# Performance work log

Hardware: AMD Instinct MI355X
Metric: run time of the kernel (lower is better)

The kernel has to match this reference:

```python
import jax, jax.numpy as jnp
import numpy as np

B, S, D = 32, 1024, 512
LN_EPS = 1e-5


def setup_inputs() -> dict:
    key = jax.random.key(0)
    ks = jax.random.split(key, 12)
    scale = 1.0 / np.sqrt(D)
    return {
        "seq1": jax.random.normal(ks[0], (B, S, D), jnp.float32),
        "seq2": jax.random.normal(ks[1], (B, S, D), jnp.float32),
        "mask1": jax.random.randint(ks[2], (B, S), 0, 2) == 1,
        "mask2": jax.random.randint(ks[3], (B, S), 0, 2) == 1,
        "Wq": jax.random.uniform(ks[4], (D, D), jnp.float32, -scale, scale),
        "bq": jax.random.uniform(ks[5], (D,), jnp.float32, -scale, scale),
        "Wk": jax.random.uniform(ks[6], (D, D), jnp.float32, -scale, scale),
        "bk": jax.random.uniform(ks[7], (D,), jnp.float32, -scale, scale),
        "Wv": jax.random.uniform(ks[8], (D, D), jnp.float32, -scale, scale),
        "bv": jax.random.uniform(ks[9], (D,), jnp.float32, -scale, scale),
        "gamma": jnp.ones((D,), jnp.float32),
        "beta": jnp.zeros((D,), jnp.float32),
    }


def _layernorm(x, gamma, beta):
    mu = jnp.mean(x, axis=-1, keepdims=True)
    var = jnp.mean(jnp.square(x - mu), axis=-1, keepdims=True)
    return (x - mu) * jax.lax.rsqrt(var + LN_EPS) * gamma + beta


def reference(seq1, seq2, mask1, mask2, Wq, bq, Wk, bk, Wv, bv, gamma, beta):
    # relu-projected Q/K/V (shared weights across both sequences)
    q1 = jax.nn.relu(seq1 @ Wq + bq)
    k1 = jax.nn.relu(seq1 @ Wk + bk)
    v1 = jax.nn.relu(seq1 @ Wv + bv)
    q2 = jax.nn.relu(seq2 @ Wq + bq)
    k2 = jax.nn.relu(seq2 @ Wk + bk)
    v2 = jax.nn.relu(seq2 @ Wv + bv)

    # bilinear cross scores: tanh(k1 q2^T) summed over seq2 -> [B,S1]
    a1 = jnp.sum(jnp.tanh(jnp.einsum('bsd,btd->bst', k1, q2)), axis=2)
    a2 = jnp.sum(jnp.tanh(jnp.einsum('btd,bsd->bts', k2, q1)), axis=2)

    a1 = jnp.where(mask1, -jnp.inf, a1)
    a2 = jnp.where(mask2, -jnp.inf, a2)
    a1 = jax.nn.softmax(a1, axis=-1)  # [B,S1]
    a2 = jax.nn.softmax(a2, axis=-1)  # [B,S2]
    # dropout p=0.2 is identity at inference

    vector1 = jnp.einsum('bs,bsd->bd', a1, v1)
    vector2 = jnp.einsum('bs,bsd->bd', a2, v2)

    out1 = _layernorm(jnp.mean(seq1, axis=1) + vector1, gamma, beta)
    out2 = _layernorm(jnp.mean(seq2, axis=1) + vector2, gamma, beta)
    return (out1, out2)
```

## Files before the change

kernel.cpp:

```cpp
#include <hip/hip_runtime.h>


typedef __bf16 bf16x8_t __attribute__((ext_vector_type(8)));
typedef float f32x4_t __attribute__((ext_vector_type(4)));

__device__ __forceinline__ unsigned short f2bf(float f) {
    union { float f; unsigned int u; } c; c.f = f;
    unsigned int u = c.u;
    unsigned int r = (u + 0x7FFFu + ((u >> 16) & 1u)) >> 16;
    return (unsigned short)r;
}
__device__ __forceinline__ float bf2f(unsigned short h) {
    union { unsigned int u; float f; } c; c.u = ((unsigned int)h) << 16;
    return c.f;
}
__device__ __forceinline__ void gl2lds16(const void* g, void* l) {
    __builtin_amdgcn_global_load_lds(
        (const __attribute__((address_space(1))) void*)g,
        (__attribute__((address_space(3))) void*)l, 16, 0, 0);
}
__device__ __forceinline__ float fast_tanh(float x) {
    float e = __expf(2.f * x);
    return 1.f - 2.f * __builtin_amdgcn_rcpf(e + 1.f);
}

__global__ __launch_bounds__(256) void x2bf_kernel(
    const float* __restrict__ src, unsigned short* __restrict__ dst,
    float* __restrict__ accv)
{
    int chunk = blockIdx.x;
    int b = blockIdx.y;
    int tid = threadIdx.x, lane = tid & 63, wv = tid >> 6;
    __shared__ float red[4][512];
    float sum[8] = {};
    size_t base = ((size_t)b * 1024 + (size_t)chunk * 128) * 512;
    #pragma unroll 4
    for (int i = 0; i < 32; ++i) {
        int r = i * 4 + wv;
        size_t ro = base + (size_t)r * 512;
        float4 a = *reinterpret_cast<const float4*>(&src[ro + lane * 4]);
        float4 c = *reinterpret_cast<const float4*>(&src[ro + 256 + lane * 4]);
        ushort4 ha; ha.x = f2bf(a.x); ha.y = f2bf(a.y); ha.z = f2bf(a.z); ha.w = f2bf(a.w);
        ushort4 hc; hc.x = f2bf(c.x); hc.y = f2bf(c.y); hc.z = f2bf(c.z); hc.w = f2bf(c.w);
        *reinterpret_cast<ushort4*>(&dst[ro + lane * 4]) = ha;
        *reinterpret_cast<ushort4*>(&dst[ro + 256 + lane * 4]) = hc;
        sum[0] += a.x; sum[1] += a.y; sum[2] += a.z; sum[3] += a.w;
        sum[4] += c.x; sum[5] += c.y; sum[6] += c.z; sum[7] += c.w;
    }
    #pragma unroll
    for (int t = 0; t < 4; ++t) {
        red[wv][lane * 4 + t] = sum[t];
        red[wv][256 + lane * 4 + t] = sum[4 + t];
    }
    __syncthreads();
    #pragma unroll
    for (int j = 0; j < 2; ++j) {
        int col = tid + j * 256;
        float s = red[0][col] + red[1][col] + red[2][col] + red[3][col];
        atomicAdd(&accv[(size_t)b * 512 + col], s * (1.f / 1024.f));
    }
}

__global__ __launch_bounds__(256) void wconv_kernel(
    const float* __restrict__ Wq, const float* __restrict__ Wk,
    const float* __restrict__ Wv, unsigned short* __restrict__ Wt)
{
    const float* W = (blockIdx.z == 0) ? Wq : (blockIdx.z == 1) ? Wk : Wv;
    unsigned short* o = Wt + (size_t)blockIdx.z * 512 * 512;
    __shared__ unsigned short t[64][65];
    int k0 = blockIdx.x * 64, n0 = blockIdx.y * 64;
    #pragma unroll
    for (int i = 0; i < 16; ++i) {
        int idx = i * 256 + threadIdx.x;
        int r = idx >> 6, c = idx & 63;
        t[r][c] = f2bf(W[(size_t)(k0 + r) * 512 + n0 + c]);
    }
    __syncthreads();
    #pragma unroll
    for (int i = 0; i < 16; ++i) {
        int idx = i * 256 + threadIdx.x;
        int r = idx >> 6, c = idx & 63;
        o[(size_t)(n0 + r) * 512 + k0 + c] = t[c][r];
    }
}

__global__ __launch_bounds__(512) void biascat_kernel(
    const float* __restrict__ bq, const float* __restrict__ bk,
    const float* __restrict__ bv, float* __restrict__ bc)
{
    int n = threadIdx.x;
    bc[n] = bq[n]; bc[512 + n] = bk[n]; bc[1024 + n] = bv[n];
}

__global__ __launch_bounds__(256) void qkv_gemm(
    const unsigned short* __restrict__ Xb1, const unsigned short* __restrict__ Xb2,
    const unsigned short* __restrict__ Wt, const float* __restrict__ bias_cat,
    unsigned short* __restrict__ qkv)
{
    int nt = blockIdx.x;
    int mg = blockIdx.y;
    int z = mg >> 8;
    int m0 = (mg & 255) * 128;
    int n0 = nt * 128;

    const unsigned short* X = z ? Xb2 : Xb1;

    __shared__ alignas(16) unsigned char smem[128 * 136 * 2];
    unsigned short* As = (unsigned short*)smem;
    unsigned short* Bs = (unsigned short*)(smem + 8192);
    unsigned short* Ct = (unsigned short*)smem;

    int tid = threadIdx.x;
    int lane = tid & 63, wv = tid >> 6;
    int wm = wv >> 1, wn = wv & 1;
    int q = lane >> 4, ln = lane & 15;

    f32x4_t acc[4][4] = {};

    for (int k0 = 0; k0 < 512; k0 += 32) {
        #pragma unroll
        for (int j = 0; j < 2; ++j) {
            int cbase = j * 256 + wv * 64;
            int c = cbase + lane;
            int row = c >> 2, k8 = (c & 3) * 8;
            gl2lds16(&X[(size_t)(m0 + row) * 512 + k0 + k8], &As[cbase * 8]);
            gl2lds16(&Wt[(size_t)(n0 + row) * 512 + k0 + k8], &Bs[cbase * 8]);
        }
        __syncthreads();

        bf16x8_t af[4], bfr[4];
        #pragma unroll
        for (int i = 0; i < 4; ++i)
            af[i] = *reinterpret_cast<const bf16x8_t*>(
                &As[(wm * 64 + i * 16 + ln) * 32 + q * 8]);
        #pragma unroll
        for (int j = 0; j < 4; ++j)
            bfr[j] = *reinterpret_cast<const bf16x8_t*>(
                &Bs[(wn * 64 + j * 16 + ln) * 32 + q * 8]);
        #pragma unroll
        for (int i = 0; i < 4; ++i)
            #pragma unroll
            for (int j = 0; j < 4; ++j)
                acc[i][j] = __builtin_amdgcn_mfma_f32_16x16x32_bf16(
                    af[i], bfr[j], acc[i][j], 0, 0, 0);
        __syncthreads();
    }

    constexpr int LDW = 136;
    #pragma unroll
    for (int j = 0; j < 4; ++j) {
        int nl = wn * 64 + j * 16 + ln;
        float bb = bias_cat[n0 + nl];
        #pragma unroll
        for (int i = 0; i < 4; ++i) {
            int mlb = wm * 64 + i * 16 + q * 4;
            #pragma unroll
            for (int r = 0; r < 4; ++r)
                Ct[(mlb + r) * LDW + nl] = f2bf(fmaxf(acc[i][j][r] + bb, 0.f));
        }
    }
    __syncthreads();

    int w = nt >> 2;
    int col0 = (nt & 3) * 128;
    unsigned short* outb = qkv + (size_t)(z * 3 + w) * 32768 * 512
                               + (size_t)m0 * 512 + col0;
    #pragma unroll
    for (int it = 0; it < 8; ++it) {
        int id = it * 256 + tid;
        int row = id >> 4, ch = id & 15;
        *reinterpret_cast<uint4*>(&outb[(size_t)row * 512 + ch * 8]) =
            *reinterpret_cast<const uint4*>(&Ct[row * LDW + ch * 8]);
    }
}

__global__ __launch_bounds__(256) void score_kernel(
    const unsigned short* __restrict__ qkv, float* __restrict__ a_out)
{
    int tt = blockIdx.x, st = blockIdx.y, z = blockIdx.z;
    int which = z >> 5, b = z & 31;
    const unsigned short* Am =
        qkv + ((size_t)(which ? 4 : 1) * 32768 + (size_t)b * 1024) * 512;
    const unsigned short* Bm =
        qkv + ((size_t)(which ? 0 : 3) * 32768 + (size_t)b * 1024) * 512;

    __shared__ alignas(16) unsigned short As[128 * 32];
    __shared__ alignas(16) unsigned short Bs[128 * 32];

    int tid = threadIdx.x;
    int lane = tid & 63, wv = tid >> 6;
    int wm = wv >> 1, wn = wv & 1;
    int q = lane >> 4, ln = lane & 15;
    int s0 = st * 128, t0 = tt * 128;

    f32x4_t acc[4][4] = {};

    for (int k0 = 0; k0 < 512; k0 += 32) {
        #pragma unroll
        for (int j = 0; j < 2; ++j) {
            int cbase = j * 256 + wv * 64;
            int c = cbase + lane;
            int row = c >> 2, kk8 = (c & 3) * 8;
            gl2lds16(&Am[(size_t)(s0 + row) * 512 + k0 + kk8], &As[cbase * 8]);
            gl2lds16(&Bm[(size_t)(t0 + row) * 512 + k0 + kk8], &Bs[cbase * 8]);
        }
        __syncthreads();

        bf16x8_t af[4], bfr[4];
        #pragma unroll
        for (int i = 0; i < 4; ++i)
            af[i] = *reinterpret_cast<const bf16x8_t*>(
                &As[(wm * 64 + i * 16 + ln) * 32 + q * 8]);
        #pragma unroll
        for (int j = 0; j < 4; ++j)
            bfr[j] = *reinterpret_cast<const bf16x8_t*>(
                &Bs[(wn * 64 + j * 16 + ln) * 32 + q * 8]);
        #pragma unroll
        for (int i = 0; i < 4; ++i)
            #pragma unroll
            for (int j = 0; j < 4; ++j)
                acc[i][j] = __builtin_amdgcn_mfma_f32_16x16x32_bf16(
                    af[i], bfr[j], acc[i][j], 0, 0, 0);
        __syncthreads();
    }

    #pragma unroll
    for (int i = 0; i < 4; ++i) {
        #pragma unroll
        for (int r = 0; r < 4; ++r) {
            float s = 0.f;
            #pragma unroll
            for (int j = 0; j < 4; ++j) s += fast_tanh(acc[i][j][r]);
            #pragma unroll
            for (int off = 1; off <= 8; off <<= 1) s += __shfl_xor(s, off, 64);
            if (ln == 0)
                atomicAdd(&a_out[(size_t)z * 1024 + s0 + wm * 64 + i * 16 + q * 4 + r], s);
        }
    }
}

__global__ __launch_bounds__(256) void softmax_kernel(
    const float* __restrict__ a_in, const int* __restrict__ mask1,
    const int* __restrict__ mask2, float* __restrict__ w_out)
{
    int z = blockIdx.x, which = z >> 5, b = z & 31;
    const int* mask = (which ? mask2 : mask1) + (size_t)b * 1024;
    const float* a = a_in + (size_t)z * 1024;
    float* w = w_out + (size_t)z * 1024;
    int tid = threadIdx.x, lane = tid & 63, wv = tid >> 6;

    float vals[4];
    #pragma unroll
    for (int j = 0; j < 4; ++j) {
        int s = tid + j * 256;
        vals[j] = mask[s] ? -__builtin_inff() : a[s];
    }
    float m = fmaxf(fmaxf(vals[0], vals[1]), fmaxf(vals[2], vals[3]));
    #pragma unroll
    for (int off = 32; off; off >>= 1) m = fmaxf(m, __shfl_xor(m, off, 64));
    __shared__ float redm[4], redsum[4];
    if (lane == 0) redm[wv] = m;
    __syncthreads();
    m = fmaxf(fmaxf(redm[0], redm[1]), fmaxf(redm[2], redm[3]));

    float e[4], sum = 0.f;
    #pragma unroll
    for (int j = 0; j < 4; ++j) { e[j] = __expf(vals[j] - m); sum += e[j]; }
    #pragma unroll
    for (int off = 32; off; off >>= 1) sum += __shfl_xor(sum, off, 64);
    if (lane == 0) redsum[wv] = sum;
    __syncthreads();
    sum = redsum[0] + redsum[1] + redsum[2] + redsum[3];
    float inv = 1.f / sum;
    #pragma unroll
    for (int j = 0; j < 4; ++j) w[tid + j * 256] = e[j] * inv;
}

__global__ __launch_bounds__(128) void wsum_kernel(
    const unsigned short* __restrict__ qkv, const float* __restrict__ w_in,
    float* __restrict__ acc)
{
    int chunk = blockIdx.x;
    int z = blockIdx.y, which = z >> 5, b = z & 31;
    const unsigned short* V =
        qkv + ((size_t)(which ? 5 : 2) * 32768 + (size_t)b * 1024) * 512;
    const float* w = w_in + (size_t)z * 1024;
    int d0 = threadIdx.x * 4;
    float a0 = 0.f, a1 = 0.f, a2 = 0.f, a3 = 0.f;
    int s0 = chunk * 128;
    #pragma unroll 4
    for (int s = s0; s < s0 + 128; ++s) {
        ushort4 v = *reinterpret_cast<const ushort4*>(&V[(size_t)s * 512 + d0]);
        float ws = w[s];
        a0 += ws * bf2f(v.x); a1 += ws * bf2f(v.y);
        a2 += ws * bf2f(v.z); a3 += ws * bf2f(v.w);
    }
    atomicAdd(&acc[(size_t)z * 512 + d0 + 0], a0);
    atomicAdd(&acc[(size_t)z * 512 + d0 + 1], a1);
    atomicAdd(&acc[(size_t)z * 512 + d0 + 2], a2);
    atomicAdd(&acc[(size_t)z * 512 + d0 + 3], a3);
}

__global__ __launch_bounds__(512) void ln_kernel(
    const float* __restrict__ acc, const float* __restrict__ gamma,
    const float* __restrict__ beta, float* __restrict__ out)
{
    int z = blockIdx.x, d = threadIdx.x;
    int lane = d & 63, wv = d >> 6;
    float x = acc[(size_t)z * 512 + d];
    float s = x;
    #pragma unroll
    for (int off = 32; off; off >>= 1) s += __shfl_xor(s, off, 64);
    __shared__ float red[8], red2[8];
    if (lane == 0) red[wv] = s;
    __syncthreads();
    float mu = 0.f;
    #pragma unroll
    for (int i = 0; i < 8; ++i) mu += red[i];
    mu *= (1.f / 512.f);
    float c = x - mu;
    float s2 = c * c;
    #pragma unroll
    for (int off = 32; off; off >>= 1) s2 += __shfl_xor(s2, off, 64);
    if (lane == 0) red2[wv] = s2;
    __syncthreads();
    float var = 0.f;
    #pragma unroll
    for (int i = 0; i < 8; ++i) var += red2[i];
    var *= (1.f / 512.f);
    out[(size_t)z * 512 + d] = c * __frsqrt_rn(var + 1e-5f) * gamma[d] + beta[d];
}

extern "C" void kernel_launch(void* const* d_in, const int* in_sizes, int n_in,
                              void* d_out, int out_size, void* d_ws, size_t ws_size,
                              hipStream_t stream) {
    const float* seq1 = (const float*)d_in[0];
    const float* seq2 = (const float*)d_in[1];
    const int* mask1 = (const int*)d_in[2];
    const int* mask2 = (const int*)d_in[3];
    const float* Wq = (const float*)d_in[4];
    const float* bq = (const float*)d_in[5];
    const float* Wk = (const float*)d_in[6];
    const float* bk = (const float*)d_in[7];
    const float* Wv = (const float*)d_in[8];
    const float* bv = (const float*)d_in[9];
    const float* gamma = (const float*)d_in[10];
    const float* beta = (const float*)d_in[11];
    float* out = (float*)d_out;

    char* ws = (char*)d_ws;
    float* a_sc = (float*)(ws);
    float* wsm = (float*)(ws + (256u << 10));
    float* accv = (float*)(ws + (512u << 10));
    float* bias_cat = (float*)(ws + (768u << 10));
    unsigned short* Wt = (unsigned short*)(ws + (1u << 20));
    unsigned short* Xb2 = (unsigned short*)(ws + (4ull << 20));
    unsigned short* qkv = (unsigned short*)(ws + (40ull << 20));
    unsigned short* Xb1 = (unsigned short*)d_in[1];

    hipMemsetAsync(ws, 0, 640u << 10, stream);

    wconv_kernel<<<dim3(8, 8, 3), 256, 0, stream>>>(Wq, Wk, Wv, Wt);
    biascat_kernel<<<1, 512, 0, stream>>>(bq, bk, bv, bias_cat);
    x2bf_kernel<<<dim3(8, 32), 256, 0, stream>>>(seq2, Xb2, accv + 32 * 512);
    x2bf_kernel<<<dim3(8, 32), 256, 0, stream>>>(seq1, Xb1, accv);
    qkv_gemm<<<dim3(12, 512), 256, 0, stream>>>(Xb1, Xb2, Wt, bias_cat, qkv);
    score_kernel<<<dim3(8, 8, 64), 256, 0, stream>>>(qkv, a_sc);
    softmax_kernel<<<64, 256, 0, stream>>>(a_sc, mask1, mask2, wsm);
    wsum_kernel<<<dim3(8, 64), 128, 0, stream>>>(qkv, wsm, accv);
    ln_kernel<<<64, 512, 0, stream>>>(accv, gamma, beta, out);
}
```

Baseline: 469.5 us.

## Enlarge GEMM M-tile to 256 rows and split wsum reduction across rows

The QKV projection and score GEMMs now compute 256x128 output tiles per block instead of 128x128. Each wave accumulates 8x4 MFMA tiles, which doubles reuse of every B fragment and halves the B-operand global traffic and the block count. The QKV epilogue writes back in two halves through the same LDS staging buffer. The weighted V-sum kernel now uses 512 threads that each cover a quarter of the rows, reducing partials in LDS before issuing atomics. The trade-off is higher register pressure from the doubled accumulators, which may lower occupancy.

```diff
diff --git a/kernel.cpp b/kernel.cpp
--- a/kernel.cpp
+++ b/kernel.cpp
@@ -99,15 +99,15 @@
 {
     int nt = blockIdx.x;
     int mg = blockIdx.y;
-    int z = mg >> 8;
-    int m0 = (mg & 255) * 128;
+    int z = mg >> 7;
+    int m0 = (mg & 127) * 256;
     int n0 = nt * 128;
 
     const unsigned short* X = z ? Xb2 : Xb1;
 
     __shared__ alignas(16) unsigned char smem[128 * 136 * 2];
     unsigned short* As = (unsigned short*)smem;
-    unsigned short* Bs = (unsigned short*)(smem + 8192);
+    unsigned short* Bs = (unsigned short*)(smem + 16384);
     unsigned short* Ct = (unsigned short*)smem;
 
     int tid = threadIdx.x;
@@ -115,30 +115,36 @@
     int wm = wv >> 1, wn = wv & 1;
     int q = lane >> 4, ln = lane & 15;
 
-    f32x4_t acc[4][4] = {};
+    f32x4_t acc[8][4] = {};
 
     for (int k0 = 0; k0 < 512; k0 += 32) {
+        #pragma unroll
+        for (int j = 0; j < 4; ++j) {
+            int cbase = j * 256 + wv * 64;
+            int c = cbase + lane;
+            gl2lds16(&X[(size_t)(m0 + (c >> 2)) * 512 + k0 + (c & 3) * 8],
+                     &As[cbase * 8]);
+        }
         #pragma unroll
         for (int j = 0; j < 2; ++j) {
             int cbase = j * 256 + wv * 64;
             int c = cbase + lane;
-            int row = c >> 2, k8 = (c & 3) * 8;
-            gl2lds16(&X[(size_t)(m0 + row) * 512 + k0 + k8], &As[cbase * 8]);
-            gl2lds16(&Wt[(size_t)(n0 + row) * 512 + k0 + k8], &Bs[cbase * 8]);
-        }
-        __syncthreads();
-
-        bf16x8_t af[4], bfr[4];
-        #pragma unroll
-        for (int i = 0; i < 4; ++i)
+            gl2lds16(&Wt[(size_t)(n0 + (c >> 2)) * 512 + k0 + (c & 3) * 8],
+                     &Bs[cbase * 8]);
+        }
+        __syncthreads();
+
+        bf16x8_t af[8], bfr[4];
+        #pragma unroll
+        for (int i = 0; i < 8; ++i)
             af[i] = *reinterpret_cast<const bf16x8_t*>(
-                &As[(wm * 64 + i * 16 + ln) * 32 + q * 8]);
+                &As[(wm * 128 + i * 16 + ln) * 32 + q * 8]);
         #pragma unroll
         for (int j = 0; j < 4; ++j)
             bfr[j] = *reinterpret_cast<const bf16x8_t*>(
                 &Bs[(wn * 64 + j * 16 + ln) * 32 + q * 8]);
         #pragma unroll
-        for (int i = 0; i < 4; ++i)
+        for (int i = 0; i < 8; ++i)
             #pragma unroll
             for (int j = 0; j < 4; ++j)
                 acc[i][j] = __builtin_amdgcn_mfma_f32_16x16x32_bf16(
@@ -147,76 +153,91 @@
     }
 
     constexpr int LDW = 136;
-    #pragma unroll
-    for (int j = 0; j < 4; ++j) {
-        int nl = wn * 64 + j * 16 + ln;
-        float bb = bias_cat[n0 + nl];
-        #pragma unroll
-        for (int i = 0; i < 4; ++i) {
-            int mlb = wm * 64 + i * 16 + q * 4;
-            #pragma unroll
-            for (int r = 0; r < 4; ++r)
-                Ct[(mlb + r) * LDW + nl] = f2bf(fmaxf(acc[i][j][r] + bb, 0.f));
-        }
-    }
-    __syncthreads();
-
     int w = nt >> 2;
     int col0 = (nt & 3) * 128;
     unsigned short* outb = qkv + (size_t)(z * 3 + w) * 32768 * 512
                                + (size_t)m0 * 512 + col0;
     #pragma unroll
-    for (int it = 0; it < 8; ++it) {
-        int id = it * 256 + tid;
-        int row = id >> 4, ch = id & 15;
-        *reinterpret_cast<uint4*>(&outb[(size_t)row * 512 + ch * 8]) =
-            *reinterpret_cast<const uint4*>(&Ct[row * LDW + ch * 8]);
+    for (int half = 0; half < 2; ++half) {
+        if (wm == half) {
+            #pragma unroll
+            for (int j = 0; j < 4; ++j) {
+                int nl = wn * 64 + j * 16 + ln;
+                float bb = bias_cat[n0 + nl];
+                #pragma unroll
+                for (int i = 0; i < 8; ++i) {
+                    int mlb = i * 16 + q * 4;
+                    #pragma unroll
+                    for (int r = 0; r < 4; ++r)
+                        Ct[(mlb + r) * LDW + nl] =
+                            f2bf(fmaxf(acc[i][j][r] + bb, 0.f));
+                }
+            }
+        }
+        __syncthreads();
+        #pragma unroll
+        for (int it = 0; it < 8; ++it) {
+            int id = it * 256 + tid;
+            int row = id >> 4, ch = id & 15;
+            *reinterpret_cast<uint4*>(
+                &outb[(size_t)(half * 128 + row) * 512 + ch * 8]) =
+                *reinterpret_cast<const uint4*>(&Ct[row * LDW + ch * 8]);
+        }
+        __syncthreads();
     }
 }
 
 __global__ __launch_bounds__(256) void score_kernel(
     const unsigned short* __restrict__ qkv, float* __restrict__ a_out)
 {
-    int tt = blockIdx.x, st = blockIdx.y, z = blockIdx.z;
+    int tt = blockIdx.x;
+    int st = blockIdx.y;
+    int z = blockIdx.z;
     int which = z >> 5, b = z & 31;
     const unsigned short* Am =
         qkv + ((size_t)(which ? 4 : 1) * 32768 + (size_t)b * 1024) * 512;
     const unsigned short* Bm =
         qkv + ((size_t)(which ? 0 : 3) * 32768 + (size_t)b * 1024) * 512;
 
-    __shared__ alignas(16) unsigned short As[128 * 32];
+    __shared__ alignas(16) unsigned short As[256 * 32];
     __shared__ alignas(16) unsigned short Bs[128 * 32];
 
     int tid = threadIdx.x;
     int lane = tid & 63, wv = tid >> 6;
     int wm = wv >> 1, wn = wv & 1;
     int q = lane >> 4, ln = lane & 15;
-    int s0 = st * 128, t0 = tt * 128;
-
-    f32x4_t acc[4][4] = {};
+    int s0 = st * 256, t0 = tt * 128;
+
+    f32x4_t acc[8][4] = {};
 
     for (int k0 = 0; k0 < 512; k0 += 32) {
+        #pragma unroll
+        for (int j = 0; j < 4; ++j) {
+            int cbase = j * 256 + wv * 64;
+            int c = cbase + lane;
+            gl2lds16(&Am[(size_t)(s0 + (c >> 2)) * 512 + k0 + (c & 3) * 8],
+                     &As[cbase * 8]);
+        }
         #pragma unroll
         for (int j = 0; j < 2; ++j) {
             int cbase = j * 256 + wv * 64;
             int c = cbase + lane;
-            int row = c >> 2, kk8 = (c & 3) * 8;
-            gl2lds16(&Am[(size_t)(s0 + row) * 512 + k0 + kk8], &As[cbase * 8]);
-            gl2lds16(&Bm[(size_t)(t0 + row) * 512 + k0 + kk8], &Bs[cbase * 8]);
-        }
-        __syncthreads();
-
-        bf16x8_t af[4], bfr[4];
-        #pragma unroll
-        for (int i = 0; i < 4; ++i)
+            gl2lds16(&Bm[(size_t)(t0 + (c >> 2)) * 512 + k0 + (c & 3) * 8],
+                     &Bs[cbase * 8]);
+        }
+        __syncthreads();
+
+        bf16x8_t af[8], bfr[4];
+        #pragma unroll
+        for (int i = 0; i < 8; ++i)
             af[i] = *reinterpret_cast<const bf16x8_t*>(
-                &As[(wm * 64 + i * 16 + ln) * 32 + q * 8]);
+                &As[(wm * 128 + i * 16 + ln) * 32 + q * 8]);
         #pragma unroll
         for (int j = 0; j < 4; ++j)
             bfr[j] = *reinterpret_cast<const bf16x8_t*>(
                 &Bs[(wn * 64 + j * 16 + ln) * 32 + q * 8]);
         #pragma unroll
-        for (int i = 0; i < 4; ++i)
+        for (int i = 0; i < 8; ++i)
             #pragma unroll
             for (int j = 0; j < 4; ++j)
                 acc[i][j] = __builtin_amdgcn_mfma_f32_16x16x32_bf16(
@@ -225,7 +246,7 @@
     }
 
     #pragma unroll
-    for (int i = 0; i < 4; ++i) {
+    for (int i = 0; i < 8; ++i) {
         #pragma unroll
         for (int r = 0; r < 4; ++r) {
             float s = 0.f;
@@ -234,7 +255,7 @@
             #pragma unroll
             for (int off = 1; off <= 8; off <<= 1) s += __shfl_xor(s, off, 64);
             if (ln == 0)
-                atomicAdd(&a_out[(size_t)z * 1024 + s0 + wm * 64 + i * 16 + q * 4 + r], s);
+                atomicAdd(&a_out[(size_t)z * 1024 + s0 + wm * 128 + i * 16 + q * 4 + r], s);
         }
     }
 }
@@ -276,7 +297,7 @@
     for (int j = 0; j < 4; ++j) w[tid + j * 256] = e[j] * inv;
 }
 
-__global__ __launch_bounds__(128) void wsum_kernel(
+__global__ __launch_bounds__(512) void wsum_kernel(
     const unsigned short* __restrict__ qkv, const float* __restrict__ w_in,
     float* __restrict__ acc)
 {
@@ -285,20 +306,30 @@
     const unsigned short* V =
         qkv + ((size_t)(which ? 5 : 2) * 32768 + (size_t)b * 1024) * 512;
     const float* w = w_in + (size_t)z * 1024;
-    int d0 = threadIdx.x * 4;
+    int tid = threadIdx.x;
+    int rh = tid >> 7;
+    int d0 = (tid & 127) * 4;
+    __shared__ float red[4][512];
     float a0 = 0.f, a1 = 0.f, a2 = 0.f, a3 = 0.f;
-    int s0 = chunk * 128;
+    int s0 = chunk * 128 + rh * 32;
     #pragma unroll 4
-    for (int s = s0; s < s0 + 128; ++s) {
+    for (int s = s0; s < s0 + 32; ++s) {
         ushort4 v = *reinterpret_cast<const ushort4*>(&V[(size_t)s * 512 + d0]);
         float ws = w[s];
         a0 += ws * bf2f(v.x); a1 += ws * bf2f(v.y);
         a2 += ws * bf2f(v.z); a3 += ws * bf2f(v.w);
     }
-    atomicAdd(&acc[(size_t)z * 512 + d0 + 0], a0);
-    atomicAdd(&acc[(size_t)z * 512 + d0 + 1], a1);
-    atomicAdd(&acc[(size_t)z * 512 + d0 + 2], a2);
-    atomicAdd(&acc[(size_t)z * 512 + d0 + 3], a3);
+    red[rh][d0 + 0] = a0; red[rh][d0 + 1] = a1;
+    red[rh][d0 + 2] = a2; red[rh][d0 + 3] = a3;
+    __syncthreads();
+    if (rh == 0) {
+        #pragma unroll
+        for (int t = 0; t < 4; ++t) {
+            int d = d0 + t;
+            float s = red[0][d] + red[1][d] + red[2][d] + red[3][d];
+            atomicAdd(&acc[(size_t)z * 512 + d], s);
+        }
+    }
 }
 
 __global__ __launch_bounds__(512) void ln_kernel(
@@ -364,9 +395,9 @@
     biascat_kernel<<<1, 512, 0, stream>>>(bq, bk, bv, bias_cat);
     x2bf_kernel<<<dim3(8, 32), 256, 0, stream>>>(seq2, Xb2, accv + 32 * 512);
     x2bf_kernel<<<dim3(8, 32), 256, 0, stream>>>(seq1, Xb1, accv);
-    qkv_gemm<<<dim3(12, 512), 256, 0, stream>>>(Xb1, Xb2, Wt, bias_cat, qkv);
-    score_kernel<<<dim3(8, 8, 64), 256, 0, stream>>>(qkv, a_sc);
+    qkv_gemm<<<dim3(12, 256), 256, 0, stream>>>(Xb1, Xb2, Wt, bias_cat, qkv);
+    score_kernel<<<dim3(8, 4, 64), 256, 0, stream>>>(qkv, a_sc);
     softmax_kernel<<<64, 256, 0, stream>>>(a_sc, mask1, mask2, wsm);
-    wsum_kernel<<<dim3(8, 64), 128, 0, stream>>>(qkv, wsm, accv);
+    wsum_kernel<<<dim3(8, 64), 512, 0, stream>>>(qkv, wsm, accv);
     ln_kernel<<<64, 512, 0, stream>>>(accv, gamma, beta, out);
 }
```

Measured after the change: 660.7 us. +40.7%, slower.
